# Performance work log

Measured on AMD Instinct MI355X. Metric: run time of the kernel, lower is better.

## Reference

```python
import jax, jax.numpy as jnp
import numpy as np

N_NODES = 50000
N_EDGES = 800000
D = 128
N_LAYERS = 4
N_GRAPHS = 512
N_CLASS = 10


def setup_inputs() -> dict:
    key = jax.random.key(0)
    ks = jax.random.split(key, 12)
    x = jax.random.normal(ks[0], (N_NODES, D), dtype=jnp.float32)
    edge_index = jax.random.randint(ks[1], (2, N_EDGES), 0, N_NODES, dtype=jnp.int64)
    batch = jnp.sort(jax.random.randint(ks[2], (N_NODES,), 0, N_GRAPHS, dtype=jnp.int64))
    s = 1.0 / np.sqrt(D)
    W_conv = jax.random.uniform(ks[3], (N_LAYERS, D, D), jnp.float32, -s, s)
    b_conv = jnp.zeros((N_LAYERS, D), jnp.float32)
    W1 = jax.random.uniform(ks[4], (D, D), jnp.float32, -s, s)
    b1 = jnp.zeros((D,), jnp.float32)
    W2 = jax.random.uniform(ks[5], (D, D // 2), jnp.float32, -s, s)
    b2 = jnp.zeros((D // 2,), jnp.float32)
    W3 = jax.random.uniform(ks[6], (D // 2, N_CLASS), jnp.float32, -1.0 / np.sqrt(D // 2), 1.0 / np.sqrt(D // 2))
    b3 = jnp.zeros((N_CLASS,), jnp.float32)
    return {"x": x, "edge_index": edge_index, "batch": batch,
            "W_conv": W_conv, "b_conv": b_conv,
            "W1": W1, "b1": b1, "W2": W2, "b2": b2, "W3": W3, "b3": b3}


def reference(x, edge_index, batch, W_conv, b_conv, W1, b1, W2, b2, W3, b3):
    row, col = edge_index[0], edge_index[1]  # messages: source=row -> target=col
    # GCN symmetric normalization with self-loops (PyG GCNConv default).
    deg = jax.ops.segment_sum(jnp.ones((row.shape[0],), x.dtype), col, num_segments=N_NODES) + 1.0
    dinv = jax.lax.rsqrt(deg)
    edge_norm = (dinv[row] * dinv[col])[:, None]      # [E,1]
    self_norm = (1.0 / deg)[:, None]                  # [N,1] = dinv_i * dinv_i

    def gcn_layer(h, W, b):
        h = h @ W                                      # [N,D]
        agg = jax.ops.segment_sum(h[row] * edge_norm, col, num_segments=N_NODES)
        agg = agg + h * self_norm                      # self-loop contribution
        return jax.nn.relu(agg + b)

    h = x
    for l in range(N_LAYERS):
        h = gcn_layer(h, W_conv[l], b_conv[l])

    # global_add_pool over graph ids
    g = jax.ops.segment_sum(h, batch, num_segments=N_GRAPHS)  # [G,D]

    # MLP head (dropout is identity in eval mode)
    g = jax.nn.relu(g @ W1 + b1)
    g = jax.nn.relu(g @ W2 + b2)
    return g @ W3 + b3
```

## Files before the change

kernel.cpp:

```cpp
#include <hip/hip_runtime.h>
#include <stdint.h>
#include <stddef.h>

#define NN 50000
#define NE 800000
#define DD 128
#define NL 4
#define NG 512
#define NC 10
#define NB 196
#define BCAP 5056
#define GPB 49

using short8 = __attribute__((ext_vector_type(8))) short;
using f32x4  = __attribute__((ext_vector_type(4))) float;

__device__ __forceinline__ float bf2f(unsigned short u) {
  union { unsigned int i; float f; } c; c.i = ((unsigned int)u) << 16; return c.f;
}
__device__ __forceinline__ unsigned short f2bf(float f) {
  union { unsigned int i; float f; } c; c.f = f;
  unsigned int i = c.i;
  return (unsigned short)((i + 0x7FFFu + ((i >> 16) & 1u)) >> 16);
}
__device__ __forceinline__ unsigned int pack2(float a, float b) {
  return (unsigned int)f2bf(a) | ((unsigned int)f2bf(b) << 16);
}
__device__ __forceinline__ void acc8(float* a, uint4 p) {
  a[0] += bf2f((unsigned short)(p.x & 0xffffu)); a[1] += bf2f((unsigned short)(p.x >> 16));
  a[2] += bf2f((unsigned short)(p.y & 0xffffu)); a[3] += bf2f((unsigned short)(p.y >> 16));
  a[4] += bf2f((unsigned short)(p.z & 0xffffu)); a[5] += bf2f((unsigned short)(p.z >> 16));
  a[6] += bf2f((unsigned short)(p.w & 0xffffu)); a[7] += bf2f((unsigned short)(p.w >> 16));
}

__global__ __launch_bounds__(1024) void p1a_k(const int* __restrict__ ecol,
                                              int* __restrict__ histM) {
  __shared__ int lh[NB];
  int tid = threadIdx.x;
  if (tid < NB) lh[tid] = 0;
  __syncthreads();
  int e0 = blockIdx.x * 4096 + tid;
#pragma unroll
  for (int j = 0; j < 4; ++j) {
    int e = e0 + j * 1024;
    if (e < NE) atomicAdd(&lh[ecol[e] >> 8], 1);
  }
  __syncthreads();
  if (tid < 256) histM[blockIdx.x * 256 + tid] = (tid < NB) ? lh[tid] : 0;
}

__global__ __launch_bounds__(256) void scanb_k(const int* __restrict__ histM,
                                               int* __restrict__ ebase,
                                               int* __restrict__ cursor,
                                               int* __restrict__ csr_ptr) {
  __shared__ int sc[256];
  int t = threadIdx.x;
  int h = 0;
  for (int b = 0; b < NB; ++b) h += histM[b * 256 + t];
  sc[t] = h; __syncthreads();
  for (int off = 1; off < 256; off <<= 1) {
    int v = (t >= off) ? sc[t - off] : 0;
    __syncthreads();
    sc[t] += v;
    __syncthreads();
  }
  if (t < NB) { ebase[t] = sc[t] - h; cursor[t] = sc[t] - h; }
  if (t == NB - 1) ebase[NB] = sc[t];
  if (t == 0) csr_ptr[NN] = NE;
}

__global__ __launch_bounds__(1024) void p1b_k(const int* __restrict__ erow,
                                              const int* __restrict__ ecol,
                                              int* __restrict__ cursor,
                                              unsigned int* __restrict__ ebuf) {
  __shared__ int lcnt[NB], gb[NB];
  int tid = threadIdx.x;
  if (tid < NB) lcnt[tid] = 0;
  __syncthreads();
  int e0 = blockIdx.x * 4096 + tid;
  int bk[4], sl[4]; unsigned int pk[4];
#pragma unroll
  for (int j = 0; j < 4; ++j) {
    int e = e0 + j * 1024;
    bk[j] = -1;
    if (e < NE) {
      int d = ecol[e], s = erow[e];
      bk[j] = d >> 8;
      pk[j] = ((unsigned int)(d & 255) << 16) | (unsigned int)s;
      sl[j] = atomicAdd(&lcnt[bk[j]], 1);
    }
  }
  __syncthreads();
  if (tid < NB) {
    int c = lcnt[tid];
    gb[tid] = c ? atomicAdd(&cursor[tid], c) : 0;
  }
  __syncthreads();
#pragma unroll
  for (int j = 0; j < 4; ++j)
    if (bk[j] >= 0) ebuf[gb[bk[j]] + sl[j]] = pk[j];
}

__global__ __launch_bounds__(1024) void p2_k(const unsigned int* __restrict__ ebuf,
                                             const int* __restrict__ ebase,
                                             const float* __restrict__ x,
                                             const int* __restrict__ batch,
                                             const float* __restrict__ Wc,
                                             int* __restrict__ csr_ptr,
                                             int* __restrict__ csr_src,
                                             float* __restrict__ dinv,
                                             unsigned short* __restrict__ xb,
                                             int* __restrict__ gptr,
                                             unsigned short* __restrict__ Wbt) {
  int b = blockIdx.x, tid = threadIdx.x;
  if (b >= NB + GPB) {
    int l = b - NB - GPB;
    const float* W = Wc + (size_t)l * DD * DD;
    unsigned short* WT = Wbt + (size_t)l * DD * DD;
    for (int i = tid; i < DD * DD; i += 1024) {
      int n = i >> 7, k = i & 127;
      WT[n * DD + k] = f2bf(W[k * DD + n]);
    }
    return;
  }
  if (b >= NB) {
    int i = (b - NB) * 1024 + tid;
    if (i >= NN) return;
    int bb = batch[i];
    int bp = (i == 0) ? -1 : batch[i - 1];
    for (int g = bp + 1; g <= bb; ++g) gptr[g] = i;
    if (i == NN - 1) { for (int g = bb + 1; g <= NG; ++g) gptr[g] = NN; }
    return;
  }

  __shared__ unsigned int pr[BCAP];
  __shared__ int srcb[BCAP];
  __shared__ int hist_s[256], scn[256], lcur[256];
  __shared__ float dinv_s[256];
  int beg = ebase[b];
  int cnt = ebase[b + 1] - beg;
  if (cnt > BCAP) cnt = BCAP;

  if (tid < 256) hist_s[tid] = 0;
  __syncthreads();
  for (int i = tid; i < cnt; i += 1024) {
    unsigned int p = ebuf[beg + i];
    pr[i] = p;
    atomicAdd(&hist_s[p >> 16], 1);
  }
  __syncthreads();
  if (tid < 256) scn[tid] = hist_s[tid];
  __syncthreads();
  for (int off = 1; off < 256; off <<= 1) {
    int v = (tid < 256 && tid >= off) ? scn[tid - off] : 0;
    __syncthreads();
    if (tid < 256) scn[tid] += v;
    __syncthreads();
  }
  if (tid < 256) {
    int ex = scn[tid] - hist_s[tid];
    lcur[tid] = ex;
    int V = b * 256 + tid;
    if (V < NN) {
      csr_ptr[V] = beg + ex;
      float dv = rsqrtf((float)(hist_s[tid] + 1));
      dinv[V] = dv;
      dinv_s[tid] = dv;
    }
  }
  __syncthreads();
  for (int i = tid; i < cnt; i += 1024) {
    unsigned int p = pr[i];
    int pos = atomicAdd(&lcur[p >> 16], 1);
    srcb[pos] = (int)(p & 0xFFFFu);
  }
  __syncthreads();
  for (int i = tid; i < cnt; i += 1024) csr_src[beg + i] = srcb[i];

  for (int i4 = tid; i4 < 256 * 32; i4 += 1024) {
    int vl = i4 >> 5;
    int V = b * 256 + vl;
    if (V < NN) {
      float d = dinv_s[vl];
      int q = i4 & 31;
      f32x4 vx = *((const f32x4*)(x + (size_t)V * DD) + q);
      uint2 o;
      o.x = pack2(vx[0] * d, vx[1] * d);
      o.y = pack2(vx[2] * d, vx[3] * d);
      ((uint2*)(xb + (size_t)V * DD))[q] = o;
    }
  }
}

__global__ __launch_bounds__(256) void agg_k(const unsigned short* __restrict__ hs,
                                             unsigned short* __restrict__ agg,
                                             const int* __restrict__ csr_ptr,
                                             const int* __restrict__ csr_src,
                                             const float* __restrict__ dinv) {
  int v = blockIdx.x * 4 + (threadIdx.x >> 6);
  if (v >= NN) return;
  int lane = threadIdx.x & 63;
  int qg = lane >> 4, r = lane & 15;
  const uint4* rows = (const uint4*)hs;

  float a[8] = {0.f, 0.f, 0.f, 0.f, 0.f, 0.f, 0.f, 0.f};
  float b[8] = {0.f, 0.f, 0.f, 0.f, 0.f, 0.f, 0.f, 0.f};
  if (qg == 0) acc8(a, rows[(size_t)v * 16 + r]);

  int e = csr_ptr[v] + qg, end = csr_ptr[v + 1];
  for (; e + 12 < end; e += 16) {
    int s0 = csr_src[e];
    int s1 = csr_src[e + 4];
    int s2 = csr_src[e + 8];
    int s3 = csr_src[e + 12];
    uint4 p0 = rows[(size_t)s0 * 16 + r];
    uint4 p1 = rows[(size_t)s1 * 16 + r];
    uint4 p2 = rows[(size_t)s2 * 16 + r];
    uint4 p3 = rows[(size_t)s3 * 16 + r];
    acc8(a, p0); acc8(b, p1); acc8(a, p2); acc8(b, p3);
  }
  for (; e + 4 < end; e += 8) {
    int s0 = csr_src[e];
    int s1 = csr_src[e + 4];
    uint4 p0 = rows[(size_t)s0 * 16 + r];
    uint4 p1 = rows[(size_t)s1 * 16 + r];
    acc8(a, p0); acc8(b, p1);
  }
  if (e < end) acc8(a, rows[(size_t)csr_src[e] * 16 + r]);

#pragma unroll
  for (int t = 0; t < 8; ++t) a[t] += b[t];

#pragma unroll
  for (int t = 0; t < 8; ++t) {
    a[t] += __shfl_xor(a[t], 16, 64);
    a[t] += __shfl_xor(a[t], 32, 64);
  }

  if (qg == 0) {
    float dv = dinv[v];
    uint4 o;
    o.x = pack2(dv * a[0], dv * a[1]);
    o.y = pack2(dv * a[2], dv * a[3]);
    o.z = pack2(dv * a[4], dv * a[5]);
    o.w = pack2(dv * a[6], dv * a[7]);
    *((uint4*)(agg + (size_t)v * DD) + r) = o;
  }
}

__global__ __launch_bounds__(256) void gemm_relu_k(const unsigned short* __restrict__ A,
                                                   const unsigned short* __restrict__ Wb,
                                                   const float* __restrict__ bias,
                                                   unsigned short* __restrict__ out,
                                                   const float* __restrict__ dscale,
                                                   int M) {
  __shared__ unsigned short Wt[128][136];
  int tid = threadIdx.x;
  for (int i = tid; i < 128 * 16; i += 256) {
    int rr = i >> 4, c = i & 15;
    *(uint4*)&Wt[rr][c * 8] = *(const uint4*)(Wb + rr * DD + c * 8);
  }
  __syncthreads();

  int wave = tid >> 6, lane = tid & 63;
  int q = lane >> 4, r = lane & 15;
  int row0 = blockIdx.x * 64 + wave * 16;

  int arow = row0 + r;
  if (arow > M - 1) arow = M - 1;
  const short* Arow = (const short*)A + (size_t)arow * DD;

  short8 afrag[4];
#pragma unroll
  for (int ks = 0; ks < 4; ++ks)
    afrag[ks] = *(const short8*)(Arow + ks * 32 + q * 8);

  f32x4 acc[8];
#pragma unroll
  for (int ct = 0; ct < 8; ++ct) acc[ct] = (f32x4){0.f, 0.f, 0.f, 0.f};

#pragma unroll
  for (int ks = 0; ks < 4; ++ks) {
#pragma unroll
    for (int ct = 0; ct < 8; ++ct) {
      short8 bfrag = *(const short8*)(&Wt[ct * 16 + r][ks * 32 + q * 8]);
      acc[ct] = __builtin_amdgcn_mfma_f32_16x16x32_bf16(afrag[ks], bfrag, acc[ct], 0, 0, 0);
    }
  }

  int orow = row0 + q * 4;
  float sc[4];
#pragma unroll
  for (int reg = 0; reg < 4; ++reg) {
    int rr = orow + reg;
    sc[reg] = (dscale && rr < M) ? dscale[rr] : 1.f;
  }
#pragma unroll
  for (int ct = 0; ct < 8; ++ct) {
    int coln = ct * 16 + r;
    float bc = bias[coln];
#pragma unroll
    for (int reg = 0; reg < 4; ++reg) {
      int rr = orow + reg;
      if (rr < M) {
        float val = fmaxf(acc[ct][reg] + bc, 0.f) * sc[reg];
        out[(size_t)rr * DD + coln] = f2bf(val);
      }
    }
  }
}

__global__ __launch_bounds__(128) void poolmlp_k(const unsigned short* __restrict__ h,
                                                 const int* __restrict__ gptr,
                                                 const float* __restrict__ W1,
                                                 const float* __restrict__ b1,
                                                 const float* __restrict__ W2,
                                                 const float* __restrict__ b2,
                                                 const float* __restrict__ W3,
                                                 const float* __restrict__ b3,
                                                 float* __restrict__ out) {
  __shared__ float s_g[128], s_h1[128], s_h2[64];
  int g = blockIdx.x, t = threadIdx.x;
  int beg = gptr[g], end = gptr[g + 1];
  float acc = 0.f;
  for (int v = beg; v < end; ++v) acc += bf2f(h[(size_t)v * DD + t]);
  s_g[t] = acc;
  __syncthreads();
  {
    float a = b1[t];
    for (int k = 0; k < 128; ++k) a += s_g[k] * W1[k * 128 + t];
    s_h1[t] = fmaxf(a, 0.f);
  }
  __syncthreads();
  if (t < 64) {
    float a = b2[t];
    for (int k = 0; k < 128; ++k) a += s_h1[k] * W2[k * 64 + t];
    s_h2[t] = fmaxf(a, 0.f);
  }
  __syncthreads();
  if (t < NC) {
    float a = b3[t];
    for (int k = 0; k < 64; ++k) a += s_h2[k] * W3[k * NC + t];
    out[g * NC + t] = a;
  }
}


extern "C" void kernel_launch(void* const* d_in, const int* in_sizes, int n_in,
                              void* d_out, int out_size, void* d_ws, size_t ws_size,
                              hipStream_t stream) {
  const float* x     = (const float*)d_in[0];
  const int*   ei    = (const int*)d_in[1];
  const int*   batch = (const int*)d_in[2];
  const float* Wc    = (const float*)d_in[3];
  const float* bc    = (const float*)d_in[4];
  const float* W1    = (const float*)d_in[5];
  const float* b1    = (const float*)d_in[6];
  const float* W2    = (const float*)d_in[7];
  const float* b2    = (const float*)d_in[8];
  const float* W3    = (const float*)d_in[9];
  const float* b3    = (const float*)d_in[10];
  float* out = (float*)d_out;

  const int* erow = ei;
  const int* ecol = ei + NE;

  char* w = (char*)d_ws;
  int*   histM   = (int*)w;    w += (size_t)NB * 256 * 4;
  int*   cursor  = (int*)w;    w += NB * 4;
  int*   ebase   = (int*)w;    w += (NB + 4) * 4;
  int*   csr_ptr = (int*)w;    w += (size_t)(NN + 4) * 4;
  int*   gptr    = (int*)w;    w += (NG + 4) * 4;
  int*   csr_src = (int*)w;    w += (size_t)NE * 4;
  float* dinv    = (float*)w;  w += (size_t)NN * 4;
  w = (char*)(((uintptr_t)w + 255) & ~(uintptr_t)255);
  unsigned short* Wbt  = (unsigned short*)w; w += (size_t)NL * DD * DD * 2;
  unsigned short* xb   = (unsigned short*)w; w += (size_t)NN * DD * 2;
  unsigned short* aggb = (unsigned short*)w; w += (size_t)NN * DD * 2;
  unsigned short* hbuf = (unsigned short*)w; w += (size_t)NN * DD * 2;
  unsigned int* ebuf = (unsigned int*)aggb;

  p1a_k  <<<NB, 1024, 0, stream>>>(ecol, histM);
  scanb_k<<<1, 256, 0, stream>>>(histM, ebase, cursor, csr_ptr);
  p1b_k  <<<NB, 1024, 0, stream>>>(erow, ecol, cursor, ebuf);
  p2_k   <<<NB + GPB + NL, 1024, 0, stream>>>(ebuf, ebase, x, batch, Wc, csr_ptr,
                                              csr_src, dinv, xb, gptr, Wbt);

  const int aggGrid  = (NN + 3) / 4;
  const int gemmGrid = (NN + 63) / 64;

  for (int l = 0; l < NL; ++l) {
    const unsigned short* hin = (l == 0) ? xb : hbuf;
    const float* dsc = (l == NL - 1) ? nullptr : dinv;
    agg_k<<<aggGrid, 256, 0, stream>>>(hin, aggb, csr_ptr, csr_src, dinv);
    gemm_relu_k<<<gemmGrid, 256, 0, stream>>>(aggb, Wbt + (size_t)l * DD * DD,
                                              bc + (size_t)l * DD, hbuf, dsc, NN);
  }

  poolmlp_k<<<NG, 128, 0, stream>>>(hbuf, gptr, W1, b1, W2, b2, W3, b3, out);

  (void)in_sizes; (void)n_in; (void)out_size; (void)ws_size;
}
```

Before: 347.8 us.

## Build CSR with fixed-capacity buckets, dropping the histogram and scan kernels

New measurement: 323.0 us. 1.08x faster.

```diff
diff --git a/kernel.cpp b/kernel.cpp
--- a/kernel.cpp
+++ b/kernel.cpp
@@ -33,42 +33,6 @@
   a[6] += bf2f((unsigned short)(p.w & 0xffffu)); a[7] += bf2f((unsigned short)(p.w >> 16));
 }
 
-__global__ __launch_bounds__(1024) void p1a_k(const int* __restrict__ ecol,
-                                              int* __restrict__ histM) {
-  __shared__ int lh[NB];
-  int tid = threadIdx.x;
-  if (tid < NB) lh[tid] = 0;
-  __syncthreads();
-  int e0 = blockIdx.x * 4096 + tid;
-#pragma unroll
-  for (int j = 0; j < 4; ++j) {
-    int e = e0 + j * 1024;
-    if (e < NE) atomicAdd(&lh[ecol[e] >> 8], 1);
-  }
-  __syncthreads();
-  if (tid < 256) histM[blockIdx.x * 256 + tid] = (tid < NB) ? lh[tid] : 0;
-}
-
-__global__ __launch_bounds__(256) void scanb_k(const int* __restrict__ histM,
-                                               int* __restrict__ ebase,
-                                               int* __restrict__ cursor,
-                                               int* __restrict__ csr_ptr) {
-  __shared__ int sc[256];
-  int t = threadIdx.x;
-  int h = 0;
-  for (int b = 0; b < NB; ++b) h += histM[b * 256 + t];
-  sc[t] = h; __syncthreads();
-  for (int off = 1; off < 256; off <<= 1) {
-    int v = (t >= off) ? sc[t - off] : 0;
-    __syncthreads();
-    sc[t] += v;
-    __syncthreads();
-  }
-  if (t < NB) { ebase[t] = sc[t] - h; cursor[t] = sc[t] - h; }
-  if (t == NB - 1) ebase[NB] = sc[t];
-  if (t == 0) csr_ptr[NN] = NE;
-}
-
 __global__ __launch_bounds__(1024) void p1b_k(const int* __restrict__ erow,
                                               const int* __restrict__ ecol,
                                               int* __restrict__ cursor,
@@ -98,15 +62,16 @@
   __syncthreads();
 #pragma unroll
   for (int j = 0; j < 4; ++j)
-    if (bk[j] >= 0) ebuf[gb[bk[j]] + sl[j]] = pk[j];
+    if (bk[j] >= 0) ebuf[(size_t)bk[j] * BCAP + gb[bk[j]] + sl[j]] = pk[j];
 }
 
 __global__ __launch_bounds__(1024) void p2_k(const unsigned int* __restrict__ ebuf,
-                                             const int* __restrict__ ebase,
+                                             const int* __restrict__ cursor,
                                              const float* __restrict__ x,
                                              const int* __restrict__ batch,
                                              const float* __restrict__ Wc,
                                              int* __restrict__ csr_ptr,
+                                             int* __restrict__ csr_end,
                                              int* __restrict__ csr_src,
                                              float* __restrict__ dinv,
                                              unsigned short* __restrict__ xb,
@@ -137,8 +102,8 @@
   __shared__ int srcb[BCAP];
   __shared__ int hist_s[256], scn[256], lcur[256];
   __shared__ float dinv_s[256];
-  int beg = ebase[b];
-  int cnt = ebase[b + 1] - beg;
+  size_t beg = (size_t)b * BCAP;
+  int cnt = cursor[b];
   if (cnt > BCAP) cnt = BCAP;
 
   if (tid < 256) hist_s[tid] = 0;
@@ -162,7 +127,8 @@
     lcur[tid] = ex;
     int V = b * 256 + tid;
     if (V < NN) {
-      csr_ptr[V] = beg + ex;
+      csr_ptr[V] = (int)beg + ex;
+      csr_end[V] = (int)beg + scn[tid];
       float dv = rsqrtf((float)(hist_s[tid] + 1));
       dinv[V] = dv;
       dinv_s[tid] = dv;
@@ -195,6 +161,7 @@
 __global__ __launch_bounds__(256) void agg_k(const unsigned short* __restrict__ hs,
                                              unsigned short* __restrict__ agg,
                                              const int* __restrict__ csr_ptr,
+                                             const int* __restrict__ csr_end,
                                              const int* __restrict__ csr_src,
                                              const float* __restrict__ dinv) {
   int v = blockIdx.x * 4 + (threadIdx.x >> 6);
@@ -207,7 +174,7 @@
   float b[8] = {0.f, 0.f, 0.f, 0.f, 0.f, 0.f, 0.f, 0.f};
   if (qg == 0) acc8(a, rows[(size_t)v * 16 + r]);
 
-  int e = csr_ptr[v] + qg, end = csr_ptr[v + 1];
+  int e = csr_ptr[v] + qg, end = csr_end[v];
   for (; e + 12 < end; e += 16) {
     int s0 = csr_src[e];
     int s1 = csr_src[e + 4];
@@ -230,7 +197,6 @@
 
 #pragma unroll
   for (int t = 0; t < 8; ++t) a[t] += b[t];
-
 #pragma unroll
   for (int t = 0; t < 8; ++t) {
     a[t] += __shfl_xor(a[t], 16, 64);
@@ -366,38 +332,39 @@
   const int* ecol = ei + NE;
 
   char* w = (char*)d_ws;
-  int*   histM   = (int*)w;    w += (size_t)NB * 256 * 4;
   int*   cursor  = (int*)w;    w += NB * 4;
-  int*   ebase   = (int*)w;    w += (NB + 4) * 4;
   int*   csr_ptr = (int*)w;    w += (size_t)(NN + 4) * 4;
+  int*   csr_end = (int*)w;    w += (size_t)(NN + 4) * 4;
   int*   gptr    = (int*)w;    w += (NG + 4) * 4;
-  int*   csr_src = (int*)w;    w += (size_t)NE * 4;
+  int*   csr_src = (int*)w;    w += (size_t)NB * BCAP * 4;
   float* dinv    = (float*)w;  w += (size_t)NN * 4;
   w = (char*)(((uintptr_t)w + 255) & ~(uintptr_t)255);
   unsigned short* Wbt  = (unsigned short*)w; w += (size_t)NL * DD * DD * 2;
   unsigned short* xb   = (unsigned short*)w; w += (size_t)NN * DD * 2;
   unsigned short* aggb = (unsigned short*)w; w += (size_t)NN * DD * 2;
-  unsigned short* hbuf = (unsigned short*)w; w += (size_t)NN * DD * 2;
-  unsigned int* ebuf = (unsigned int*)aggb;
-
-  p1a_k  <<<NB, 1024, 0, stream>>>(ecol, histM);
-  scanb_k<<<1, 256, 0, stream>>>(histM, ebase, cursor, csr_ptr);
-  p1b_k  <<<NB, 1024, 0, stream>>>(erow, ecol, cursor, ebuf);
-  p2_k   <<<NB + GPB + NL, 1024, 0, stream>>>(ebuf, ebase, x, batch, Wc, csr_ptr,
-                                              csr_src, dinv, xb, gptr, Wbt);
+  unsigned short* hA   = (unsigned short*)w; w += (size_t)NN * DD * 2;
+  unsigned short* hB   = (unsigned short*)w; w += (size_t)NN * DD * 2;
+  unsigned int* ebuf = (unsigned int*)hA;
+
+  hipMemsetAsync(cursor, 0, NB * 4, stream);
+
+  p1b_k<<<NB, 1024, 0, stream>>>(erow, ecol, cursor, ebuf);
+  p2_k <<<NB + GPB + NL, 1024, 0, stream>>>(ebuf, cursor, x, batch, Wc, csr_ptr,
+                                            csr_end, csr_src, dinv, xb, gptr, Wbt);
 
   const int aggGrid  = (NN + 3) / 4;
   const int gemmGrid = (NN + 63) / 64;
 
   for (int l = 0; l < NL; ++l) {
-    const unsigned short* hin = (l == 0) ? xb : hbuf;
+    const unsigned short* hin = (l == 0) ? xb : ((l & 1) ? hA : hB);
+    unsigned short* dst = (l & 1) ? hB : hA;
     const float* dsc = (l == NL - 1) ? nullptr : dinv;
-    agg_k<<<aggGrid, 256, 0, stream>>>(hin, aggb, csr_ptr, csr_src, dinv);
+    agg_k<<<aggGrid, 256, 0, stream>>>(hin, aggb, csr_ptr, csr_end, csr_src, dinv);
     gemm_relu_k<<<gemmGrid, 256, 0, stream>>>(aggb, Wbt + (size_t)l * DD * DD,
-                                              bc + (size_t)l * DD, hbuf, dsc, NN);
-  }
-
-  poolmlp_k<<<NG, 128, 0, stream>>>(hbuf, gptr, W1, b1, W2, b2, W3, b3, out);
+                                              bc + (size_t)l * DD, dst, dsc, NN);
+  }
+
+  poolmlp_k<<<NG, 128, 0, stream>>>(hB, gptr, W1, b1, W2, b2, W3, b3, out);
 
   (void)in_sizes; (void)n_in; (void)out_size; (void)ws_size;
 }
```
